# Kernel optimization log

Hardware: AMD Instinct MI355X
Metric: run time of the kernel (lower is better)

## Reference

```python
import jax, jax.numpy as jnp
import numpy as np

B, N, FD, D, HF, WF = 4, 6, 256, 128, 64, 120
IMG_H, IMG_W = 480, 960
EPS_LN = 1e-5


def bilinear_sample(fmap, pts):
    """fmap: (B,C,H,W); pts: (B,P,2) xy pixel coords. Returns (B,P,C) values
    (zeros padding, align_corners=True convention) and (B,P) in-bounds mask."""
    Bc, C, H, W = fmap.shape
    flat = fmap.reshape(Bc, C, H * W)
    x, y = pts[..., 0], pts[..., 1]
    x0, y0 = jnp.floor(x), jnp.floor(y)
    out = jnp.zeros((Bc, pts.shape[1], C), fmap.dtype)
    for dx in (0.0, 1.0):
        for dy in (0.0, 1.0):
            cx, cy = x0 + dx, y0 + dy
            wgt = (1.0 - jnp.abs(x - cx)) * (1.0 - jnp.abs(y - cy))
            inb = (cx >= 0) & (cx <= W - 1) & (cy >= 0) & (cy <= H - 1)
            idx = (jnp.clip(cy, 0, H - 1) * W + jnp.clip(cx, 0, W - 1)).astype(jnp.int32)
            g = jnp.take_along_axis(flat, idx[:, None, :], axis=2)  # (B,C,P)
            out = out + (g * (wgt * inb)[:, None, :]).transpose(0, 2, 1)
    valid = (x >= 0) & (x <= W - 1) & (y >= 0) & (y <= H - 1)
    return out, valid


def _l2norm(x, axis):
    n = jnp.sqrt(jnp.sum(x * x, axis=axis, keepdims=True))
    return x / jnp.maximum(n, 1e-12)


def _ln(x, g, b):
    mu = jnp.mean(x, axis=-1, keepdims=True)
    var = jnp.mean((x - mu) ** 2, axis=-1, keepdims=True)
    return (x - mu) / jnp.sqrt(var + EPS_LN) * g + b


def setup_inputs() -> dict:
    key = jax.random.key(0)
    ks = jax.random.split(key, 12)
    rng = np.random.RandomState(0)
    feature = jax.random.normal(ks[0], (B, N, FD, HF, WF), jnp.float32)
    # realistic intrinsics (same K family for src/tar so homographies land in-frame)
    K = np.zeros((B, N, 3, 3), np.float32)
    K[..., 0, 0] = IMG_W * 0.8 * (1 + 0.01 * rng.randn(B, N))
    K[..., 1, 1] = IMG_W * 0.8 * (1 + 0.01 * rng.randn(B, N))
    K[..., 0, 2] = IMG_W / 2
    K[..., 1, 2] = IMG_H / 2
    K[..., 2, 2] = 1.0
    I_tar_inv = np.linalg.inv(K[:, 0]).astype(np.float32)  # (B,3,3)
    # extrinsics: near-identity rotation + small translation
    E = np.tile(np.eye(4, dtype=np.float32), (B, N, 1, 1))
    w = 0.02 * rng.randn(B, N, 3).astype(np.float32)
    skew = np.zeros((B, N, 3, 3), np.float32)
    skew[..., 0, 1], skew[..., 0, 2] = -w[..., 2], w[..., 1]
    skew[..., 1, 0], skew[..., 1, 2] = w[..., 2], -w[..., 0]
    skew[..., 2, 0], skew[..., 2, 1] = -w[..., 1], w[..., 0]
    E[..., :3, :3] = np.eye(3, dtype=np.float32) + skew
    E[..., :3, 3] = 0.1 * rng.randn(B, N, 3).astype(np.float32)
    nv = np.tile(np.array([0.0, -1.0, 0.0], np.float32), (B, 1, 1))
    nv += 0.01 * rng.randn(B, 1, 3).astype(np.float32)
    nv /= np.linalg.norm(nv, axis=-1, keepdims=True)
    sc_in, sc_hid = 1.0 / np.sqrt(FD), 1.0 / np.sqrt(D)
    return {
        "feature": feature,
        "I_src": jnp.asarray(K),
        "I_tar_inv": jnp.asarray(I_tar_inv),
        "E": jnp.asarray(E),
        "dis": jnp.float32(1.5),
        "norm_vec": jnp.asarray(nv),
        "bn_gamma": jnp.ones((FD,), jnp.float32),
        "bn_beta": jnp.zeros((FD,), jnp.float32),
        "bn_mean": jnp.zeros((FD,), jnp.float32),
        "bn_var": jnp.ones((FD,), jnp.float32),
        "conv_w": jax.random.normal(ks[1], (D, FD), jnp.float32) * sc_in,
        "ln1_g": jnp.ones((D,), jnp.float32),
        "ln1_b": jnp.zeros((D,), jnp.float32),
        "mlp_w1": jax.random.normal(ks[2], (D, 2 * D), jnp.float32) * sc_hid,
        "mlp_b1": jnp.zeros((2 * D,), jnp.float32),
        "mlp_w2": jax.random.normal(ks[3], (2 * D, D), jnp.float32) * sc_hid,
        "mlp_b2": jnp.zeros((D,), jnp.float32),
        "ln2_g": jnp.ones((D,), jnp.float32),
        "ln2_b": jnp.zeros((D,), jnp.float32),
    }


def reference(feature, I_src, I_tar_inv, E, dis, norm_vec, bn_gamma, bn_beta,
              bn_mean, bn_var, conv_w, ln1_g, ln1_b, mlp_w1, mlp_b1, mlp_w2,
              mlp_b2, ln2_g, ln2_b):
    b, n, fd, h, w = feature.shape
    d = conv_w.shape[0]
    P = h * w
    # feature_linear: BN (inference stats) + ReLU + 1x1 conv (no bias)
    f = (feature - bn_mean[:, None, None]) / jnp.sqrt(bn_var[:, None, None] + 1e-5)
    f = f * bn_gamma[:, None, None] + bn_beta[:, None, None]
    f = jax.nn.relu(f)
    val = jnp.einsum('of,bnfhw->bnohw', conv_w, f)  # (b,n,d,h,w)
    # homography of normalized grid scaled to image pixels
    xs = jnp.linspace(0.0, 1.0, w)
    ys = jnp.linspace(0.0, 1.0, h)
    X, Y = jnp.meshgrid(xs, ys)  # (h,w), xy indexing
    pix = jnp.stack([X.ravel() * IMG_W, Y.ravel() * IMG_H, jnp.ones(P)], 0)  # (3,P)
    R = E[..., :3, :3]
    T = E[..., :3, 3:]
    Hm = I_src @ (R - (T @ norm_vec[:, None]) / dis) @ I_tar_inv[:, None]  # (b,n,3,3)
    homo = jnp.einsum('bnij,jp->bnip', Hm, pix.astype(Hm.dtype))
    uv = homo[:, :, :2] / homo[:, :, 2:3]
    uv = uv / jnp.array([[IMG_W], [IMG_H]], uv.dtype)  # (b,n,2,P) in ~[0,1]
    # HomoGuideAttention
    pts = (uv * jnp.array([[w], [h]], uv.dtype)).transpose(0, 1, 3, 2).reshape(b * n, P, 2)
    sampled, valid = bilinear_sample(val.reshape(b * n, d, h, w), pts)  # (bn,P,d),(bn,P)
    keyv = _l2norm(sampled, axis=2).reshape(b, n, P, d)
    query = val[:, 0]  # (b,d,h,w)
    q = _l2norm(query.reshape(b, d, P), axis=1)
    dot = jnp.einsum('bdp,bnpd->bnp', q, keyv)
    dot = dot * valid.reshape(b, n, P).astype(dot.dtype)
    att = jax.nn.softmax(dot, axis=1)
    z = jnp.einsum('bnp,bnpd->bpd', att, sampled.reshape(b, n, P, d))
    z = z.transpose(0, 2, 1).reshape(b, d, h, w) + query
    z = z.reshape(b, d, P).transpose(0, 2, 1)  # (b,P,d)
    z = _ln(z, ln1_g, ln1_b)
    hmid = jax.nn.gelu(z @ mlp_w1 + mlp_b1, approximate=False)
    z = z + (hmid @ mlp_w2 + mlp_b2)
    z = _ln(z, ln2_g, ln2_b)
    return z.transpose(0, 2, 1).reshape(b, d, h, w)
```

## Files before the change

### kernel.cpp

```cpp
#include <hip/hip_runtime.h>
#include <hip/hip_bf16.h>
#include <math.h>

#define B_ 4
#define N_ 6
#define FD_ 256
#define D_ 128
#define HF_ 64
#define WF_ 120
#define P_ (HF_*WF_)

typedef __attribute__((ext_vector_type(8))) short short8;
typedef __attribute__((ext_vector_type(4))) float floatx4;
typedef __attribute__((ext_vector_type(4))) unsigned int uint4e;

__device__ inline float gred_sum(float v) {
  v += __shfl_xor(v, 1); v += __shfl_xor(v, 2);
  v += __shfl_xor(v, 4); v += __shfl_xor(v, 8);
  return v;
}

__device__ inline unsigned short f2bf(float f) {
  unsigned int u = __builtin_bit_cast(unsigned int, f);
  u += 0x7fffu + ((u >> 16) & 1u);
  return (unsigned short)(u >> 16);
}
__device__ inline float bf2f(unsigned short h) {
  return __builtin_bit_cast(float, ((unsigned int)h) << 16);
}
__device__ inline void bfu2(unsigned int u, float& lo, float& hi) {
  lo = __builtin_bit_cast(float, u << 16);
  hi = __builtin_bit_cast(float, u & 0xffff0000u);
}

__global__ void prep_kernel(const float* __restrict__ I_src, const float* __restrict__ I_tar_inv,
                            const float* __restrict__ E, const float* __restrict__ dis,
                            const float* __restrict__ norm_vec,
                            const float* __restrict__ bn_gamma, const float* __restrict__ bn_beta,
                            const float* __restrict__ bn_mean, const float* __restrict__ bn_var,
                            float* __restrict__ bnscale, float* __restrict__ bnbias,
                            float* __restrict__ Hm) {
  int t = threadIdx.x;
  if (t < FD_) {
    float s = bn_gamma[t] * rsqrtf(bn_var[t] + 1e-5f);
    bnscale[t] = s;
    bnbias[t] = bn_beta[t] - bn_mean[t] * s;
  }
  if (t < B_*N_) {
    int b = t / N_;
    const float* e = E + t*16;
    const float* nv = norm_vec + b*3;
    float inv_dis = 1.0f / dis[0];
    float M[9];
    #pragma unroll
    for (int r = 0; r < 3; r++)
      #pragma unroll
      for (int c = 0; c < 3; c++)
        M[r*3+c] = e[r*4+c] - e[r*4+3]*nv[c]*inv_dis;
    const float* Is = I_src + t*9;
    float A[9];
    #pragma unroll
    for (int r = 0; r < 3; r++)
      #pragma unroll
      for (int c = 0; c < 3; c++)
        A[r*3+c] = Is[r*3+0]*M[0*3+c] + Is[r*3+1]*M[1*3+c] + Is[r*3+2]*M[2*3+c];
    const float* It = I_tar_inv + b*9;
    #pragma unroll
    for (int r = 0; r < 3; r++)
      #pragma unroll
      for (int c = 0; c < 3; c++)
        Hm[t*9 + r*3+c] = A[r*3+0]*It[0*3+c] + A[r*3+1]*It[1*3+c] + A[r*3+2]*It[2*3+c];
  }
}

__global__ void uv_kernel(const float* __restrict__ Hm, float2* __restrict__ uvbuf) {
  int t = blockIdx.x * 256 + threadIdx.x;
  int p  = t % P_;
  int bn = t / P_;
  int py = p / WF_, px = p - py*WF_;
  float pixx = (float)px * (960.f/119.f);
  float pixy = (float)py * (480.f/63.f);
  const float* H = Hm + bn*9;
  float hx = H[0]*pixx + H[1]*pixy + H[2];
  float hy = H[3]*pixx + H[4]*pixy + H[5];
  float hz = H[6]*pixx + H[7]*pixy + H[8];
  float sx = (hx/hz) * ((float)WF_/960.f);
  float sy = (hy/hz) * ((float)HF_/480.f);
  uvbuf[t] = make_float2(sx, sy);
}

__global__ void swizzle_w_kernel(const float* __restrict__ conv_w, unsigned short* __restrict__ wswz) {
  int t = blockIdx.x * 256 + threadIdx.x;
  int j    =  t        & 7;
  int lane = (t >> 3)  & 63;
  int dt   = (t >> 9)  & 7;
  int kc   =  t >> 12;
  int d = dt*16 + (lane & 15);
  int k = kc*32 + (lane >> 4)*8 + j;
  wswz[t] = f2bf(conv_w[d*FD_ + k]);
}

__global__ void swizzle_mlp_kernel(const float* __restrict__ w1, const float* __restrict__ w2,
                                   unsigned short* __restrict__ w1s, unsigned short* __restrict__ w2s) {
  int t = blockIdx.x * 256 + threadIdx.x;
  if (t < 32768) {
    int j    =  t        & 7;
    int lane = (t >> 3)  & 63;
    int dt   = (t >> 9)  & 15;
    int kc   =  t >> 13;
    int n = dt*16 + (lane & 15);
    int k = kc*32 + (lane >> 4)*8 + j;
    w1s[t] = f2bf(w1[k*256 + n]);
  } else {
    int u = t - 32768;
    int j    =  u        & 7;
    int lane = (u >> 3)  & 63;
    int dt   = (u >> 9)  & 7;
    int kc   =  u >> 12;
    int n = dt*16 + (lane & 15);
    int k = kc*32 + (lane >> 4)*8 + j;
    w2s[u] = f2bf(w2[k*128 + n]);
  }
}

#define AST_ 36
__global__ __launch_bounds__(256) void conv_kernel(const float* __restrict__ feature,
    const unsigned short* __restrict__ wswz, const float* __restrict__ bnscale,
    const float* __restrict__ bnbias, unsigned short* __restrict__ val) {
  __shared__ __align__(16) char csm[19968];
  unsigned short* apadA = (unsigned short*)csm;
  unsigned short* apadB = (unsigned short*)(csm + 4608);
  unsigned short* ytile = (unsigned short*)csm;
  float* sbn = (float*)(csm + 17408);

  int tid = threadIdx.x;
  sbn[tid] = bnscale[tid]; sbn[256+tid] = bnbias[tid];

  int bn = blockIdx.y;
  int p0 = blockIdx.x * 64;
  const float* fbase2 = feature + (size_t)bn*FD_*P_ + p0;

  int K0 = tid >> 4;
  int sp = (tid & 15) * 4;

  int ln = tid & 63, wv = tid >> 6;
  int m = ln & 15, q = ln >> 4;
  int row = wv*16 + m;

  float4 va[2], vb[2];
  {
    const float* fb0 = fbase2 + (size_t)(2*K0)*P_ + sp;
    va[0] = *(const float4*)fb0; vb[0] = *(const float4*)(fb0 + P_);
    const float* fb1 = fbase2 + (size_t)(32 + 2*K0)*P_ + sp;
    va[1] = *(const float4*)fb1; vb[1] = *(const float4*)(fb1 + P_);
  }
  __syncthreads();

  floatx4 acc[8];
  #pragma unroll
  for (int dt = 0; dt < 8; dt++) acc[dt] = (floatx4){0.f,0.f,0.f,0.f};

  {
    int k0 = 0;
    float s0 = sbn[k0+2*K0],   b0 = sbn[256+k0+2*K0];
    float s1 = sbn[k0+2*K0+1], b1 = sbn[256+k0+2*K0+1];
    float a0[4] = {va[0].x, va[0].y, va[0].z, va[0].w};
    float a1[4] = {vb[0].x, vb[0].y, vb[0].z, vb[0].w};
    #pragma unroll
    for (int i = 0; i < 4; i++) {
      unsigned int w = (unsigned int)f2bf(fmaxf(a0[i]*s0+b0, 0.f))
                     | ((unsigned int)f2bf(fmaxf(a1[i]*s1+b1, 0.f)) << 16);
      *(unsigned int*)&apadA[(sp+i)*AST_ + 2*K0] = w;
    }
  }

  #pragma unroll
  for (int kc = 0; kc < 8; kc++) {
    __syncthreads();
    if (kc + 2 < 8) {
      const float* fb = fbase2 + (size_t)((kc+2)*32 + 2*K0)*P_ + sp;
      va[kc&1] = *(const float4*)fb;
      vb[kc&1] = *(const float4*)(fb + P_);
    }
    if (kc + 1 < 8) {
      int s = (kc+1)&1;
      int k0 = (kc+1)*32;
      unsigned short* ap = ((kc+1)&1) ? apadB : apadA;
      float s0 = sbn[k0+2*K0],   b0 = sbn[256+k0+2*K0];
      float s1 = sbn[k0+2*K0+1], b1 = sbn[256+k0+2*K0+1];
      float a0[4] = {va[s].x, va[s].y, va[s].z, va[s].w};
      float a1[4] = {vb[s].x, vb[s].y, vb[s].z, vb[s].w};
      #pragma unroll
      for (int i = 0; i < 4; i++) {
        unsigned int w = (unsigned int)f2bf(fmaxf(a0[i]*s0+b0, 0.f))
                       | ((unsigned int)f2bf(fmaxf(a1[i]*s1+b1, 0.f)) << 16);
        *(unsigned int*)&ap[(sp+i)*AST_ + 2*K0] = w;
      }
    }
    unsigned short* rp = (kc&1) ? apadB : apadA;
    uint2 u0 = *(const uint2*)&rp[row*AST_ + q*8];
    uint2 u1 = *(const uint2*)&rp[row*AST_ + q*8 + 4];
    uint4e ua = {u0.x, u0.y, u1.x, u1.y};
    short8 af = __builtin_bit_cast(short8, ua);
    #pragma unroll
    for (int dt = 0; dt < 8; dt++) {
      short8 bfg = *(const short8*)(wswz + (((size_t)kc*8 + dt)*64 + ln)*8);
      acc[dt] = __builtin_amdgcn_mfma_f32_16x16x32_bf16(af, bfg, acc[dt], 0, 0, 0);
    }
  }
  __syncthreads();

  #pragma unroll
  for (int dt = 0; dt < 8; dt++)
    #pragma unroll
    for (int r = 0; r < 4; r++)
      ytile[(wv*16 + q*4 + r)*136 + dt*16 + m] = f2bf(acc[dt][r]);
  __syncthreads();
  #pragma unroll
  for (int i = 0; i < 4; i++) {
    int idx = tid + i*256;
    int pp = idx >> 4, ch = idx & 15;
    uint4 v = *(const uint4*)&ytile[pp*136 + ch*8];
    *(uint4*)(val + ((size_t)bn*P_ + p0 + pp)*D_ + ch*8) = v;
  }
}

__global__ __launch_bounds__(256) void att_kernel(const unsigned short* __restrict__ val,
    const float2* __restrict__ uvbuf, const float* __restrict__ ln1_g,
    const float* __restrict__ ln1_b, unsigned short* __restrict__ zbuf) {
  int b = blockIdx.y;
  int p0 = blockIdx.x * 32;
  int tid = threadIdx.x;
  int ln = tid & 63, wv = tid >> 6;
  int grp = ln >> 4, c = ln & 15;

  float g1[8], be1[8];
  *(float4*)&g1[0]  = *(const float4*)(ln1_g + c*8);
  *(float4*)&g1[4]  = *(const float4*)(ln1_g + c*8 + 4);
  *(float4*)&be1[0] = *(const float4*)(ln1_b + c*8);
  *(float4*)&be1[4] = *(const float4*)(ln1_b + c*8 + 4);

  for (int pi = 0; pi < 2; pi++) {
    int p = p0 + wv*8 + grp*2 + pi;

    uint4 qu = *(const uint4*)(val + ((size_t)(b*N_)*P_ + p)*D_ + c*8);
    float qv[8];
    bfu2(qu.x, qv[0], qv[1]); bfu2(qu.y, qv[2], qv[3]);
    bfu2(qu.z, qv[4], qv[5]); bfu2(qu.w, qv[6], qv[7]);
    float qp = 0.f;
    #pragma unroll
    for (int i = 0; i < 8; i++) qp += qv[i]*qv[i];
    float qinv = 1.f / fmaxf(sqrtf(gred_sum(qp)), 1e-12f);

    float dotv[N_];
    float sv[N_][8];
    #pragma unroll
    for (int np = 0; np < 3; np++) {
      uint4 g[2][4]; float wm[2][4]; bool vld[2];
      #pragma unroll
      for (int t = 0; t < 2; t++) {
        int n = np*2 + t;
        float2 uv = uvbuf[((size_t)(b*N_ + n))*P_ + p];
        float sx = uv.x, sy = uv.y;
        float x0f = floorf(sx), y0f = floorf(sy);
        float fx = sx - x0f, fy = sy - y0f;
        int x0 = (int)x0f, y0 = (int)y0f;
        const unsigned short* base = val + ((size_t)(b*N_+n)*P_)*D_ + c*8;
        #pragma unroll
        for (int k = 0; k < 4; k++) {
          int dx = k & 1, dy = k >> 1;
          int cx = x0 + dx, cy = y0 + dy;
          bool inb = (cx >= 0) && (cx <= WF_-1) && (cy >= 0) && (cy <= HF_-1);
          int icx = min(max(cx,0),WF_-1), icy = min(max(cy,0),HF_-1);
          wm[t][k] = inb ? (dx ? fx : 1.f-fx) * (dy ? fy : 1.f-fy) : 0.f;
          g[t][k] = *(const uint4*)(base + (size_t)(icy*WF_ + icx)*D_);
        }
        vld[t] = (sx >= 0.f) && (sx <= (float)(WF_-1)) && (sy >= 0.f) && (sy <= (float)(HF_-1));
      }
      #pragma unroll
      for (int t = 0; t < 2; t++) {
        int n = np*2 + t;
        float acc[8];
        #pragma unroll
        for (int i = 0; i < 8; i++) acc[i] = 0.f;
        #pragma unroll
        for (int k = 0; k < 4; k++) {
          float gg[8];
          bfu2(g[t][k].x, gg[0], gg[1]); bfu2(g[t][k].y, gg[2], gg[3]);
          bfu2(g[t][k].z, gg[4], gg[5]); bfu2(g[t][k].w, gg[6], gg[7]);
          float w = wm[t][k];
          #pragma unroll
          for (int i = 0; i < 8; i++) acc[i] += gg[i]*w;
        }
        float ssp = 0.f, qsp = 0.f;
        #pragma unroll
        for (int i = 0; i < 8; i++) { ssp += acc[i]*acc[i]; qsp += qv[i]*acc[i]; }
        float ss = gred_sum(ssp);
        float qs = gred_sum(qsp);
        float dn = qs * qinv / fmaxf(sqrtf(ss), 1e-12f);
        dotv[n] = vld[t] ? dn : 0.f;
        #pragma unroll
        for (int i = 0; i < 8; i++) sv[n][i] = acc[i];
      }
    }
    float mx = dotv[0];
    #pragma unroll
    for (int n = 1; n < N_; n++) mx = fmaxf(mx, dotv[n]);
    float e[N_]; float den = 0.f;
    #pragma unroll
    for (int n = 0; n < N_; n++) { e[n] = expf(dotv[n]-mx); den += e[n]; }
    float rden = 1.f/den;
    float z[8];
    #pragma unroll
    for (int i = 0; i < 8; i++) z[i] = qv[i];
    #pragma unroll
    for (int n = 0; n < N_; n++) {
      float a = e[n]*rden;
      #pragma unroll
      for (int i = 0; i < 8; i++) z[i] += a*sv[n][i];
    }
    float sp = 0.f;
    #pragma unroll
    for (int i = 0; i < 8; i++) sp += z[i];
    float mu = gred_sum(sp) * (1.f/128.f);
    float vp = 0.f;
    #pragma unroll
    for (int i = 0; i < 8; i++) { float d0 = z[i]-mu; vp += d0*d0; }
    float rs = rsqrtf(gred_sum(vp) * (1.f/128.f) + 1e-5f);
    unsigned int ow[4];
    #pragma unroll
    for (int i = 0; i < 4; i++) {
      float o0 = (z[2*i]-mu)*rs*g1[2*i] + be1[2*i];
      float o1 = (z[2*i+1]-mu)*rs*g1[2*i+1] + be1[2*i+1];
      ow[i] = (unsigned int)f2bf(o0) | ((unsigned int)f2bf(o1) << 16);
    }
    *(uint4*)(zbuf + ((size_t)b*P_ + p)*D_ + c*8) = make_uint4(ow[0], ow[1], ow[2], ow[3]);
  }
}

__global__ __launch_bounds__(256) void mlp_kernel(const unsigned short* __restrict__ zbuf,
    const unsigned short* __restrict__ w1s, const float* __restrict__ b1,
    const unsigned short* __restrict__ w2s, const float* __restrict__ b2,
    const float* __restrict__ ln2_g, const float* __restrict__ ln2_b,
    float* __restrict__ out) {
  __shared__ __align__(16) char smem[26112];
  unsigned short* zt = (unsigned short*)smem;
  unsigned short* ht = (unsigned short*)(smem + 8704);
  float* lnp = (float*)(smem + 25600);
  float* yt = (float*)smem;

  int tid = threadIdx.x;
  int b = blockIdx.y;
  int p0 = blockIdx.x * 32;
  int ln = tid & 63, wv = tid >> 6;
  int m = ln & 15, q = ln >> 4;
  int h = wv >> 1, ch2 = wv & 1;

  #pragma unroll
  for (int i = 0; i < 2; i++) {
    int idx = tid + i*256;
    int pp = idx >> 4, ch = idx & 15;
    *(uint4*)&zt[pp*136 + ch*8] = *(const uint4*)(zbuf + ((size_t)b*P_ + p0 + pp)*D_ + ch*8);
  }
  __syncthreads();

  floatx4 a1[8];
  #pragma unroll
  for (int j = 0; j < 8; j++) a1[j] = (floatx4){0.f,0.f,0.f,0.f};
  #pragma unroll
  for (int kc = 0; kc < 4; kc++) {
    short8 af = *(const short8*)&zt[(h*16+m)*136 + kc*32 + q*8];
    #pragma unroll
    for (int j = 0; j < 8; j++) {
      int dt = ch2*8 + j;
      short8 bfg = *(const short8*)(w1s + (((size_t)kc*16 + dt)*64 + ln)*8);
      a1[j] = __builtin_amdgcn_mfma_f32_16x16x32_bf16(af, bfg, a1[j], 0, 0, 0);
    }
  }
  #pragma unroll
  for (int j = 0; j < 8; j++) {
    int dt = ch2*8 + j;
    float bb = b1[dt*16 + m];
    #pragma unroll
    for (int r = 0; r < 4; r++) {
      float x = a1[j][r] + bb;
      float hv = 0.5f*x*(1.f + erff(x*0.70710678118654752f));
      ht[(h*16 + q*4 + r)*264 + dt*16 + m] = f2bf(hv);
    }
  }
  __syncthreads();

  floatx4 a2[4];
  #pragma unroll
  for (int j = 0; j < 4; j++) a2[j] = (floatx4){0.f,0.f,0.f,0.f};
  #pragma unroll
  for (int kc = 0; kc < 8; kc++) {
    short8 af = *(const short8*)&ht[(h*16+m)*264 + kc*32 + q*8];
    #pragma unroll
    for (int j = 0; j < 4; j++) {
      int dt = ch2*4 + j;
      short8 bfg = *(const short8*)(w2s + (((size_t)kc*8 + dt)*64 + ln)*8);
      a2[j] = __builtin_amdgcn_mfma_f32_16x16x32_bf16(af, bfg, a2[j], 0, 0, 0);
    }
  }
  float y[4][4];
  #pragma unroll
  for (int j = 0; j < 4; j++) {
    int dt = ch2*4 + j;
    float bb = b2[dt*16 + m];
    #pragma unroll
    for (int r = 0; r < 4; r++) {
      int pp = h*16 + q*4 + r;
      y[j][r] = a2[j][r] + bb + bf2f(zt[pp*136 + dt*16 + m]);
    }
  }
  #pragma unroll
  for (int r = 0; r < 4; r++) {
    float sp = 0.f, sq = 0.f;
    #pragma unroll
    for (int j = 0; j < 4; j++) { sp += y[j][r]; sq += y[j][r]*y[j][r]; }
    sp = gred_sum(sp); sq = gred_sum(sq);
    if (m == 0) {
      int pl = h*16 + q*4 + r;
      lnp[(ch2*32 + pl)*2 + 0] = sp;
      lnp[(ch2*32 + pl)*2 + 1] = sq;
    }
  }
  __syncthreads();
  float mu_[4], rs_[4];
  #pragma unroll
  for (int r = 0; r < 4; r++) {
    int pl = h*16 + q*4 + r;
    float sum = lnp[pl*2]     + lnp[(32+pl)*2];
    float ssq = lnp[pl*2 + 1] + lnp[(32+pl)*2 + 1];
    float mu = sum * (1.f/128.f);
    float var = fmaxf(ssq * (1.f/128.f) - mu*mu, 0.f);
    mu_[r] = mu; rs_[r] = rsqrtf(var + 1e-5f);
  }
  float gg[4], be[4];
  #pragma unroll
  for (int j = 0; j < 4; j++) {
    int d = (ch2*4 + j)*16 + m;
    gg[j] = ln2_g[d]; be[j] = ln2_b[d];
  }
  #pragma unroll
  for (int j = 0; j < 4; j++)
    #pragma unroll
    for (int r = 0; r < 4; r++)
      y[j][r] = (y[j][r] - mu_[r])*rs_[r]*gg[j] + be[j];
  __syncthreads();
  #pragma unroll
  for (int j = 0; j < 4; j++)
    #pragma unroll
    for (int r = 0; r < 4; r++)
      yt[((ch2*4 + j)*16 + m)*34 + h*16 + q*4 + r] = y[j][r];
  __syncthreads();

  #pragma unroll
  for (int i = 0; i < 8; i++) {
    int idx = tid + i*256;
    int d = idx >> 4, pu = idx & 15;
    *(float2*)(out + ((size_t)(b*D_ + d))*P_ + p0 + pu*2) = *(float2*)&yt[d*34 + pu*2];
  }
}

extern "C" void kernel_launch(void* const* d_in, const int* in_sizes, int n_in,
                              void* d_out, int out_size, void* d_ws, size_t ws_size,
                              hipStream_t stream) {
  (void)in_sizes; (void)n_in; (void)out_size; (void)ws_size;
  const float* feature   = (const float*)d_in[0];
  const float* I_src     = (const float*)d_in[1];
  const float* I_tar_inv = (const float*)d_in[2];
  const float* E         = (const float*)d_in[3];
  const float* dis       = (const float*)d_in[4];
  const float* norm_vec  = (const float*)d_in[5];
  const float* bn_gamma  = (const float*)d_in[6];
  const float* bn_beta   = (const float*)d_in[7];
  const float* bn_mean   = (const float*)d_in[8];
  const float* bn_var    = (const float*)d_in[9];
  const float* conv_w    = (const float*)d_in[10];
  const float* ln1_g     = (const float*)d_in[11];
  const float* ln1_b     = (const float*)d_in[12];
  const float* mlp_w1    = (const float*)d_in[13];
  const float* mlp_b1    = (const float*)d_in[14];
  const float* mlp_w2    = (const float*)d_in[15];
  const float* mlp_b2    = (const float*)d_in[16];
  const float* ln2_g     = (const float*)d_in[17];
  const float* ln2_b     = (const float*)d_in[18];
  float* out = (float*)d_out;

  char* ws = (char*)d_ws;
  float* bnscale       = (float*)(ws + 0);
  float* bnbias        = (float*)(ws + 1024);
  float* Hm            = (float*)(ws + 2048);
  unsigned short* wswz = (unsigned short*)(ws + 4096);
  unsigned short* w1s  = (unsigned short*)(ws + 69632);
  unsigned short* w2s  = (unsigned short*)(ws + 135168);
  float2* uvbuf        = (float2*)(ws + 200704);
  unsigned short* val  = (unsigned short*)(ws + 1675264);
  unsigned short* zbuf = (unsigned short*)(ws + 1675264 + 47185920ULL);

  hipLaunchKernelGGL(prep_kernel, dim3(1), dim3(256), 0, stream,
                     I_src, I_tar_inv, E, dis, norm_vec,
                     bn_gamma, bn_beta, bn_mean, bn_var, bnscale, bnbias, Hm);
  hipLaunchKernelGGL(uv_kernel, dim3(720), dim3(256), 0, stream, Hm, uvbuf);
  hipLaunchKernelGGL(swizzle_w_kernel, dim3(128), dim3(256), 0, stream, conv_w, wswz);
  hipLaunchKernelGGL(swizzle_mlp_kernel, dim3(256), dim3(256), 0, stream,
                     mlp_w1, mlp_w2, w1s, w2s);
  hipLaunchKernelGGL(conv_kernel, dim3(120, 24), dim3(256), 0, stream,
                     feature, wswz, bnscale, bnbias, val);
  hipLaunchKernelGGL(att_kernel, dim3(240, 4), dim3(256), 0, stream,
                     val, uvbuf, ln1_g, ln1_b, zbuf);
  hipLaunchKernelGGL(mlp_kernel, dim3(240, 4), dim3(256), 0, stream,
                     zbuf, w1s, mlp_b1, w2s, mlp_b2, ln2_g, ln2_b, out);
}
```

Measured before the change: 369.6 us.

## Spread attention gather across more threads per pixel with swizzled tile order

The attention kernel now gives each pixel 32 lanes holding 4 channels each, instead of 16 lanes holding 8 channels and two pixels per lane group in a loop. It launches four times as many blocks of 8 pixels, remaps block index to tile with a stride-120 interleave, and adds a launch-bounds occupancy hint. The aim is more memory-level parallelism and lower register pressure for the latency-bound bilinear gathers, plus possibly better cache locality across concurrently running blocks. The cost is narrower 8-byte loads and an extra shuffle step in each reduction.

```diff
diff --git a/kernel.cpp b/kernel.cpp
--- a/kernel.cpp
+++ b/kernel.cpp
@@ -17,6 +17,13 @@
 __device__ inline float gred_sum(float v) {
   v += __shfl_xor(v, 1); v += __shfl_xor(v, 2);
   v += __shfl_xor(v, 4); v += __shfl_xor(v, 8);
+  return v;
+}
+
+__device__ inline float gred32(float v) {
+  v += __shfl_xor(v, 1); v += __shfl_xor(v, 2);
+  v += __shfl_xor(v, 4); v += __shfl_xor(v, 8);
+  v += __shfl_xor(v, 16);
   return v;
 }
 
@@ -225,117 +232,112 @@
   }
 }
 
-__global__ __launch_bounds__(256) void att_kernel(const unsigned short* __restrict__ val,
+__global__ __launch_bounds__(256, 4) void att_kernel(const unsigned short* __restrict__ val,
     const float2* __restrict__ uvbuf, const float* __restrict__ ln1_g,
     const float* __restrict__ ln1_b, unsigned short* __restrict__ zbuf) {
   int b = blockIdx.y;
-  int p0 = blockIdx.x * 32;
+  int bx = blockIdx.x;
+  int tile = (bx & 7) * 120 + (bx >> 3);
+  int p0 = tile * 8;
   int tid = threadIdx.x;
   int ln = tid & 63, wv = tid >> 6;
-  int grp = ln >> 4, c = ln & 15;
-
-  float g1[8], be1[8];
-  *(float4*)&g1[0]  = *(const float4*)(ln1_g + c*8);
-  *(float4*)&g1[4]  = *(const float4*)(ln1_g + c*8 + 4);
-  *(float4*)&be1[0] = *(const float4*)(ln1_b + c*8);
-  *(float4*)&be1[4] = *(const float4*)(ln1_b + c*8 + 4);
-
-  for (int pi = 0; pi < 2; pi++) {
-    int p = p0 + wv*8 + grp*2 + pi;
-
-    uint4 qu = *(const uint4*)(val + ((size_t)(b*N_)*P_ + p)*D_ + c*8);
-    float qv[8];
-    bfu2(qu.x, qv[0], qv[1]); bfu2(qu.y, qv[2], qv[3]);
-    bfu2(qu.z, qv[4], qv[5]); bfu2(qu.w, qv[6], qv[7]);
-    float qp = 0.f;
-    #pragma unroll
-    for (int i = 0; i < 8; i++) qp += qv[i]*qv[i];
-    float qinv = 1.f / fmaxf(sqrtf(gred_sum(qp)), 1e-12f);
-
-    float dotv[N_];
-    float sv[N_][8];
-    #pragma unroll
-    for (int np = 0; np < 3; np++) {
-      uint4 g[2][4]; float wm[2][4]; bool vld[2];
-      #pragma unroll
-      for (int t = 0; t < 2; t++) {
-        int n = np*2 + t;
-        float2 uv = uvbuf[((size_t)(b*N_ + n))*P_ + p];
-        float sx = uv.x, sy = uv.y;
-        float x0f = floorf(sx), y0f = floorf(sy);
-        float fx = sx - x0f, fy = sy - y0f;
-        int x0 = (int)x0f, y0 = (int)y0f;
-        const unsigned short* base = val + ((size_t)(b*N_+n)*P_)*D_ + c*8;
+  int grp = ln >> 5, c = ln & 31;
+  int p = p0 + wv*2 + grp;
+
+  float g1[4], be1[4];
+  *(float4*)&g1[0]  = *(const float4*)(ln1_g + c*4);
+  *(float4*)&be1[0] = *(const float4*)(ln1_b + c*4);
+
+  uint2 qu = *(const uint2*)(val + ((size_t)(b*N_)*P_ + p)*D_ + c*4);
+  float qv[4];
+  bfu2(qu.x, qv[0], qv[1]); bfu2(qu.y, qv[2], qv[3]);
+  float qp = 0.f;
+  #pragma unroll
+  for (int i = 0; i < 4; i++) qp += qv[i]*qv[i];
+  float qinv = 1.f / fmaxf(sqrtf(gred32(qp)), 1e-12f);
+
+  float dotv[N_];
+  float sv[N_][4];
+  #pragma unroll
+  for (int np = 0; np < 3; np++) {
+    uint2 g[2][4]; float wm[2][4]; bool vld[2];
+    #pragma unroll
+    for (int t = 0; t < 2; t++) {
+      int n = np*2 + t;
+      float2 uv = uvbuf[((size_t)(b*N_ + n))*P_ + p];
+      float sx = uv.x, sy = uv.y;
+      float x0f = floorf(sx), y0f = floorf(sy);
+      float fx = sx - x0f, fy = sy - y0f;
+      int x0 = (int)x0f, y0 = (int)y0f;
+      const unsigned short* base = val + ((size_t)(b*N_+n)*P_)*D_ + c*4;
+      #pragma unroll
+      for (int k = 0; k < 4; k++) {
+        int dx = k & 1, dy = k >> 1;
+        int cx = x0 + dx, cy = y0 + dy;
+        bool inb = (cx >= 0) && (cx <= WF_-1) && (cy >= 0) && (cy <= HF_-1);
+        int icx = min(max(cx,0),WF_-1), icy = min(max(cy,0),HF_-1);
+        wm[t][k] = inb ? (dx ? fx : 1.f-fx) * (dy ? fy : 1.f-fy) : 0.f;
+        g[t][k] = *(const uint2*)(base + (size_t)(icy*WF_ + icx)*D_);
+      }
+      vld[t] = (sx >= 0.f) && (sx <= (float)(WF_-1)) && (sy >= 0.f) && (sy <= (float)(HF_-1));
+    }
+    #pragma unroll
+    for (int t = 0; t < 2; t++) {
+      int n = np*2 + t;
+      float acc[4];
+      #pragma unroll
+      for (int i = 0; i < 4; i++) acc[i] = 0.f;
+      #pragma unroll
+      for (int k = 0; k < 4; k++) {
+        float gg[4];
+        bfu2(g[t][k].x, gg[0], gg[1]); bfu2(g[t][k].y, gg[2], gg[3]);
+        float w = wm[t][k];
         #pragma unroll
-        for (int k = 0; k < 4; k++) {
-          int dx = k & 1, dy = k >> 1;
-          int cx = x0 + dx, cy = y0 + dy;
-          bool inb = (cx >= 0) && (cx <= WF_-1) && (cy >= 0) && (cy <= HF_-1);
-          int icx = min(max(cx,0),WF_-1), icy = min(max(cy,0),HF_-1);
-          wm[t][k] = inb ? (dx ? fx : 1.f-fx) * (dy ? fy : 1.f-fy) : 0.f;
-          g[t][k] = *(const uint4*)(base + (size_t)(icy*WF_ + icx)*D_);
-        }
-        vld[t] = (sx >= 0.f) && (sx <= (float)(WF_-1)) && (sy >= 0.f) && (sy <= (float)(HF_-1));
+        for (int i = 0; i < 4; i++) acc[i] += gg[i]*w;
       }
-      #pragma unroll
-      for (int t = 0; t < 2; t++) {
-        int n = np*2 + t;
-        float acc[8];
-        #pragma unroll
-        for (int i = 0; i < 8; i++) acc[i] = 0.f;
-        #pragma unroll
-        for (int k = 0; k < 4; k++) {
-          float gg[8];
-          bfu2(g[t][k].x, gg[0], gg[1]); bfu2(g[t][k].y, gg[2], gg[3]);
-          bfu2(g[t][k].z, gg[4], gg[5]); bfu2(g[t][k].w, gg[6], gg[7]);
-          float w = wm[t][k];
-          #pragma unroll
-          for (int i = 0; i < 8; i++) acc[i] += gg[i]*w;
-        }
-        float ssp = 0.f, qsp = 0.f;
-        #pragma unroll
-        for (int i = 0; i < 8; i++) { ssp += acc[i]*acc[i]; qsp += qv[i]*acc[i]; }
-        float ss = gred_sum(ssp);
-        float qs = gred_sum(qsp);
-        float dn = qs * qinv / fmaxf(sqrtf(ss), 1e-12f);
-        dotv[n] = vld[t] ? dn : 0.f;
-        #pragma unroll
-        for (int i = 0; i < 8; i++) sv[n][i] = acc[i];
-      }
-    }
-    float mx = dotv[0];
-    #pragma unroll
-    for (int n = 1; n < N_; n++) mx = fmaxf(mx, dotv[n]);
-    float e[N_]; float den = 0.f;
-    #pragma unroll
-    for (int n = 0; n < N_; n++) { e[n] = expf(dotv[n]-mx); den += e[n]; }
-    float rden = 1.f/den;
-    float z[8];
-    #pragma unroll
-    for (int i = 0; i < 8; i++) z[i] = qv[i];
-    #pragma unroll
-    for (int n = 0; n < N_; n++) {
-      float a = e[n]*rden;
-      #pragma unroll
-      for (int i = 0; i < 8; i++) z[i] += a*sv[n][i];
-    }
-    float sp = 0.f;
-    #pragma unroll
-    for (int i = 0; i < 8; i++) sp += z[i];
-    float mu = gred_sum(sp) * (1.f/128.f);
-    float vp = 0.f;
-    #pragma unroll
-    for (int i = 0; i < 8; i++) { float d0 = z[i]-mu; vp += d0*d0; }
-    float rs = rsqrtf(gred_sum(vp) * (1.f/128.f) + 1e-5f);
-    unsigned int ow[4];
-    #pragma unroll
-    for (int i = 0; i < 4; i++) {
-      float o0 = (z[2*i]-mu)*rs*g1[2*i] + be1[2*i];
-      float o1 = (z[2*i+1]-mu)*rs*g1[2*i+1] + be1[2*i+1];
-      ow[i] = (unsigned int)f2bf(o0) | ((unsigned int)f2bf(o1) << 16);
-    }
-    *(uint4*)(zbuf + ((size_t)b*P_ + p)*D_ + c*8) = make_uint4(ow[0], ow[1], ow[2], ow[3]);
-  }
+      float ssp = 0.f, qsp = 0.f;
+      #pragma unroll
+      for (int i = 0; i < 4; i++) { ssp += acc[i]*acc[i]; qsp += qv[i]*acc[i]; }
+      float ss = gred32(ssp);
+      float qs = gred32(qsp);
+      float dn = qs * qinv / fmaxf(sqrtf(ss), 1e-12f);
+      dotv[n] = vld[t] ? dn : 0.f;
+      #pragma unroll
+      for (int i = 0; i < 4; i++) sv[n][i] = acc[i];
+    }
+  }
+  float mx = dotv[0];
+  #pragma unroll
+  for (int n = 1; n < N_; n++) mx = fmaxf(mx, dotv[n]);
+  float e[N_]; float den = 0.f;
+  #pragma unroll
+  for (int n = 0; n < N_; n++) { e[n] = expf(dotv[n]-mx); den += e[n]; }
+  float rden = 1.f/den;
+  float z[4];
+  #pragma unroll
+  for (int i = 0; i < 4; i++) z[i] = qv[i];
+  #pragma unroll
+  for (int n = 0; n < N_; n++) {
+    float a = e[n]*rden;
+    #pragma unroll
+    for (int i = 0; i < 4; i++) z[i] += a*sv[n][i];
+  }
+  float sp = 0.f;
+  #pragma unroll
+  for (int i = 0; i < 4; i++) sp += z[i];
+  float mu = gred32(sp) * (1.f/128.f);
+  float vp = 0.f;
+  #pragma unroll
+  for (int i = 0; i < 4; i++) { float d0 = z[i]-mu; vp += d0*d0; }
+  float rs = rsqrtf(gred32(vp) * (1.f/128.f) + 1e-5f);
+  unsigned int ow[2];
+  #pragma unroll
+  for (int i = 0; i < 2; i++) {
+    float o0 = (z[2*i]-mu)*rs*g1[2*i] + be1[2*i];
+    float o1 = (z[2*i+1]-mu)*rs*g1[2*i+1] + be1[2*i+1];
+    ow[i] = (unsigned int)f2bf(o0) | ((unsigned int)f2bf(o1) << 16);
+  }
+  *(uint2*)(zbuf + ((size_t)b*P_ + p)*D_ + c*4) = make_uint2(ow[0], ow[1]);
 }
 
 __global__ __launch_bounds__(256) void mlp_kernel(const unsigned short* __restrict__ zbuf,
@@ -509,7 +511,7 @@
                      mlp_w1, mlp_w2, w1s, w2s);
   hipLaunchKernelGGL(conv_kernel, dim3(120, 24), dim3(256), 0, stream,
                      feature, wswz, bnscale, bnbias, val);
-  hipLaunchKernelGGL(att_kernel, dim3(240, 4), dim3(256), 0, stream,
+  hipLaunchKernelGGL(att_kernel, dim3(960, 4), dim3(256), 0, stream,
                      val, uvbuf, ln1_g, ln1_b, zbuf);
   hipLaunchKernelGGL(mlp_kernel, dim3(240, 4), dim3(256), 0, stream,
                      zbuf, w1s, mlp_b1, w2s, mlp_b2, ln2_g, ln2_b, out);
```

Result: faster. 359.9 us (-2.6%).
